# Kernel optimization log

Hardware: AMD Instinct MI355X
Metric: run time of the kernel (lower is better)

Reference implementation:

```python
import jax, jax.numpy as jnp
import numpy as np

N_TIME, N_BATCH, N_STATE, N_FORCE = 64, 8192, 32, 16
DT = 0.05          # implicit (backward-Euler) step size
NEWTON_ITERS = 6   # fixed Newton-Raphson iteration count (converges well below fp32 eps here)


def setup_inputs() -> dict:
    key = jax.random.key(0)
    k = jax.random.split(key, 5)
    return {
        "y0": jax.random.normal(k[0], (N_BATCH, N_STATE), jnp.float32) * 0.1,
        "forces": jax.random.normal(k[1], (N_TIME, N_BATCH, N_FORCE), jnp.float32),
        "W": jax.random.normal(k[2], (N_STATE, N_STATE), jnp.float32) / np.float32(np.sqrt(N_STATE)),
        "U": jax.random.normal(k[3], (N_STATE, N_FORCE), jnp.float32) / np.float32(np.sqrt(N_FORCE)),
        "b": jax.random.normal(k[4], (N_STATE,), jnp.float32) * 0.01,
        "n": N_TIME,
    }


def reference(y0, forces, W, U, b, n):
    """Sequential recursive nonlinear solve, block_size=1, ZeroPredictor guess.

    Each step solves R(y_k) = y_k - y_{k-1} - dt*tanh(W y_k + U u_k + b) = 0
    via Newton-Raphson with a batched dense solve of the diagonal Jacobian
    block J[1] = I - dt*diag(1-t^2) W (the Thomas factorization for a single
    step reduces to this dense solve).
    """
    S = y0.shape[-1]
    I = jnp.eye(S, dtype=y0.dtype)

    def step(y_prev, u):
        fu = u @ U.T + b                      # [B,S] constant per Newton solve
        y = jnp.zeros_like(y_prev)            # ZeroPredictor initial guess
        for _ in range(NEWTON_ITERS):         # plain Newton-Raphson
            t = jnp.tanh(y @ W.T + fu)        # [B,S]
            R = y - y_prev - DT * t           # residual [B,S]
            J = I - DT * ((1.0 - t * t)[..., :, None] * W)  # [B,S,S] dR/dy
            y = y - jnp.linalg.solve(J, R[..., None])[..., 0]
        return y, y

    _, ys = jax.lax.scan(step, y0, forces[1:n])   # sequential recursion over time
    return jnp.concatenate([y0[None], ys], axis=0)  # result[0] = y0
```

## Files before the change

kernel.cpp:

```cpp
#include <hip/hip_runtime.h>

#define NT 64
#define NB 8192
#define NS 32
#define NF 16
#define DT 0.05f

typedef float f32x4 __attribute__((ext_vector_type(4)));
typedef short s16x8 __attribute__((ext_vector_type(8)));

__device__ __forceinline__ void bsplit(float v, unsigned short& hi, unsigned short& lo) {
    unsigned int u = __float_as_uint(v);
    hi = (unsigned short)(u >> 16);
    float rest = v - __uint_as_float(u & 0xFFFF0000u);
    lo = (unsigned short)(__float_as_uint(rest) >> 16);
}

__device__ __forceinline__ void split8(const float* p, s16x8& hi, s16x8& lo) {
#pragma unroll
    for (int e = 0; e < 8; ++e) {
        unsigned short hs, ls;
        bsplit(p[e], hs, ls);
        hi[e] = (short)hs;
        lo[e] = (short)ls;
    }
}

__device__ __forceinline__ float tanh1(float x) {
    const float K = 2.8853900817779268f;
    float e = __builtin_amdgcn_exp2f(K * x);
    float r = __builtin_amdgcn_rcpf(e + 1.0f);
    return fmaf(-2.0f, r, 1.0f);
}

__global__ __launch_bounds__(64) void rnes_kernel(
    const float* __restrict__ y0,
    const float* __restrict__ forces,
    const float* __restrict__ W,
    const float* __restrict__ U,
    const float* __restrict__ bias,
    float* __restrict__ out)
{
    const int lane = threadIdx.x;
    const int m    = lane & 15;
    const int h    = lane >> 4;
    const int gb   = blockIdx.x * 16 + m;

    __shared__ __align__(16) unsigned short Yhi[16 * 40];
    __shared__ __align__(16) unsigned short Ylo[16 * 40];

    s16x8 WA0h, WA0l, WA1h, WA1l;
    split8(W + m * NS + 8 * h,        WA0h, WA0l);
    split8(W + (m + 16) * NS + 8 * h, WA1h, WA1l);

    s16x8 UA0h = {0,0,0,0,0,0,0,0}, UA0l = UA0h, UA1h = UA0h, UA1l = UA0h;
    if (h < 2) {
        split8(U + m * NF + 8 * h,        UA0h, UA0l);
        split8(U + (m + 16) * NF + 8 * h, UA1h, UA1l);
    }

    const f32x4 biasA = *(const f32x4*)(bias + 4 * h);
    const f32x4 biasB = *(const f32x4*)(bias + 16 + 4 * h);

    const float* yb = y0 + (size_t)gb * NS;
    f32x4 ypA = *(const f32x4*)(yb + 4 * h);
    f32x4 ypB = *(const f32x4*)(yb + 16 + 4 * h);
    {
        float* o0 = out + (size_t)gb * NS;
        __builtin_nontemporal_store(ypA, (f32x4*)(o0 + 4 * h));
        __builtin_nontemporal_store(ypB, (f32x4*)(o0 + 16 + 4 * h));
    }
    f32x4 yppA = ypA, yppB = ypB;

    const size_t fstep = (size_t)NB * NF;
    const float* fba = forces + (size_t)gb * NF + 8 * h;
    f32x4 un0 = {0.f,0.f,0.f,0.f}, un1 = un0;
    if (h < 2) {
        un0 = __builtin_nontemporal_load((const f32x4*)(fba + fstep));
        un1 = __builtin_nontemporal_load((const f32x4*)(fba + fstep + 4));
    }

    for (int k = 1; k < NT; ++k) {
        s16x8 Buh = {0,0,0,0,0,0,0,0}, Bul = Buh;
        if (h < 2) {
            float uv[8] = {un0[0],un0[1],un0[2],un0[3],un1[0],un1[1],un1[2],un1[3]};
            split8(uv, Buh, Bul);
        }
        f32x4 fuA = biasA;
        fuA = __builtin_amdgcn_mfma_f32_16x16x32_bf16(UA0l, Buh, fuA, 0, 0, 0);
        fuA = __builtin_amdgcn_mfma_f32_16x16x32_bf16(UA0h, Bul, fuA, 0, 0, 0);
        fuA = __builtin_amdgcn_mfma_f32_16x16x32_bf16(UA0h, Buh, fuA, 0, 0, 0);
        f32x4 fuB = biasB;
        fuB = __builtin_amdgcn_mfma_f32_16x16x32_bf16(UA1l, Buh, fuB, 0, 0, 0);
        fuB = __builtin_amdgcn_mfma_f32_16x16x32_bf16(UA1h, Bul, fuB, 0, 0, 0);
        fuB = __builtin_amdgcn_mfma_f32_16x16x32_bf16(UA1h, Buh, fuB, 0, 0, 0);

        if (h < 2) {
            int kn = (k + 1 < NT) ? (k + 1) : (NT - 1);
            un0 = __builtin_nontemporal_load((const f32x4*)(fba + (size_t)kn * fstep));
            un1 = __builtin_nontemporal_load((const f32x4*)(fba + (size_t)kn * fstep + 4));
        }

        f32x4 yA = ypA + (ypA - yppA);
        f32x4 yB = ypB + (ypB - yppB);

        auto iterate = [&]() {
            unsigned dh0, dh1, dl0, dl1;
            {
                unsigned short h0,h1,h2,h3,l0,l1,l2,l3;
                bsplit(yA[0],h0,l0); bsplit(yA[1],h1,l1);
                bsplit(yA[2],h2,l2); bsplit(yA[3],h3,l3);
                dh0 = (unsigned)h0 | ((unsigned)h1 << 16);
                dh1 = (unsigned)h2 | ((unsigned)h3 << 16);
                dl0 = (unsigned)l0 | ((unsigned)l1 << 16);
                dl1 = (unsigned)l2 | ((unsigned)l3 << 16);
            }
            *reinterpret_cast<unsigned long long*>(&Yhi[m * 40 + 4 * h]) =
                (unsigned long long)dh0 | ((unsigned long long)dh1 << 32);
            *reinterpret_cast<unsigned long long*>(&Ylo[m * 40 + 4 * h]) =
                (unsigned long long)dl0 | ((unsigned long long)dl1 << 32);
            {
                unsigned short h0,h1,h2,h3,l0,l1,l2,l3;
                bsplit(yB[0],h0,l0); bsplit(yB[1],h1,l1);
                bsplit(yB[2],h2,l2); bsplit(yB[3],h3,l3);
                dh0 = (unsigned)h0 | ((unsigned)h1 << 16);
                dh1 = (unsigned)h2 | ((unsigned)h3 << 16);
                dl0 = (unsigned)l0 | ((unsigned)l1 << 16);
                dl1 = (unsigned)l2 | ((unsigned)l3 << 16);
            }
            *reinterpret_cast<unsigned long long*>(&Yhi[m * 40 + 16 + 4 * h]) =
                (unsigned long long)dh0 | ((unsigned long long)dh1 << 32);
            *reinterpret_cast<unsigned long long*>(&Ylo[m * 40 + 16 + 4 * h]) =
                (unsigned long long)dl0 | ((unsigned long long)dl1 << 32);
            asm volatile("" ::: "memory");

            s16x8 Bh = *reinterpret_cast<const s16x8*>(&Yhi[m * 40 + 8 * h]);
            s16x8 Bl = *reinterpret_cast<const s16x8*>(&Ylo[m * 40 + 8 * h]);

            f32x4 zA = fuA;
            zA = __builtin_amdgcn_mfma_f32_16x16x32_bf16(WA0l, Bh, zA, 0, 0, 0);
            zA = __builtin_amdgcn_mfma_f32_16x16x32_bf16(WA0h, Bl, zA, 0, 0, 0);
            zA = __builtin_amdgcn_mfma_f32_16x16x32_bf16(WA0h, Bh, zA, 0, 0, 0);
            f32x4 zB = fuB;
            zB = __builtin_amdgcn_mfma_f32_16x16x32_bf16(WA1l, Bh, zB, 0, 0, 0);
            zB = __builtin_amdgcn_mfma_f32_16x16x32_bf16(WA1h, Bl, zB, 0, 0, 0);
            zB = __builtin_amdgcn_mfma_f32_16x16x32_bf16(WA1h, Bh, zB, 0, 0, 0);

#pragma unroll
            for (int r = 0; r < 4; ++r) {
                yA[r] = fmaf(DT, tanh1(zA[r]), ypA[r]);
                yB[r] = fmaf(DT, tanh1(zB[r]), ypB[r]);
            }
        };
        iterate();
        iterate();
        if (k == 1) iterate();

        yppA = ypA; yppB = ypB;
        ypA = yA;   ypB = yB;

        float* op = out + ((size_t)k * NB + gb) * NS;
        __builtin_nontemporal_store(yA, (f32x4*)(op + 4 * h));
        __builtin_nontemporal_store(yB, (f32x4*)(op + 16 + 4 * h));
    }
}

extern "C" void kernel_launch(void* const* d_in, const int* in_sizes, int n_in,
                              void* d_out, int out_size, void* d_ws, size_t ws_size,
                              hipStream_t stream) {
    const float* y0     = (const float*)d_in[0];
    const float* forces = (const float*)d_in[1];
    const float* W      = (const float*)d_in[2];
    const float* U      = (const float*)d_in[3];
    const float* b      = (const float*)d_in[4];
    float* out = (float*)d_out;

    dim3 grid(NB / 16);
    dim3 block(64);
    rnes_kernel<<<grid, block, 0, stream>>>(y0, forces, W, U, b, out);
}
```

Baseline: 152.1 us.

## Permute W/U rows so MFMA output feeds next B operand in registers

Reorders the rows of W and U assigned to each MFMA output tile so that each lane's accumulator outputs correspond exactly to the 8 contiguous state elements it needs as the B operand of the next Newton iteration. This removes the per-iteration LDS round-trip (stores of hi/lo bf16 splits plus reads) from the serial dependency chain. Output stores and bias loads are remapped to match the new element ownership. It also adds a launch bound of one block per SM hint.

```diff
diff --git a/kernel.cpp b/kernel.cpp
--- a/kernel.cpp
+++ b/kernel.cpp
@@ -33,7 +33,7 @@
     return fmaf(-2.0f, r, 1.0f);
 }
 
-__global__ __launch_bounds__(64) void rnes_kernel(
+__global__ __launch_bounds__(64, 1) void rnes_kernel(
     const float* __restrict__ y0,
     const float* __restrict__ forces,
     const float* __restrict__ W,
@@ -46,29 +46,29 @@
     const int h    = lane >> 4;
     const int gb   = blockIdx.x * 16 + m;
 
-    __shared__ __align__(16) unsigned short Yhi[16 * 40];
-    __shared__ __align__(16) unsigned short Ylo[16 * 40];
+    const int rA = 8 * (m >> 2) + (m & 3);
+    const int rB = rA + 4;
 
-    s16x8 WA0h, WA0l, WA1h, WA1l;
-    split8(W + m * NS + 8 * h,        WA0h, WA0l);
-    split8(W + (m + 16) * NS + 8 * h, WA1h, WA1l);
+    s16x8 WAh, WAl, WBh, WBl;
+    split8(W + rA * NS + 8 * h, WAh, WAl);
+    split8(W + rB * NS + 8 * h, WBh, WBl);
 
-    s16x8 UA0h = {0,0,0,0,0,0,0,0}, UA0l = UA0h, UA1h = UA0h, UA1l = UA0h;
+    s16x8 UAh = {0,0,0,0,0,0,0,0}, UAl = UAh, UBh = UAh, UBl = UAh;
     if (h < 2) {
-        split8(U + m * NF + 8 * h,        UA0h, UA0l);
-        split8(U + (m + 16) * NF + 8 * h, UA1h, UA1l);
+        split8(U + rA * NF + 8 * h, UAh, UAl);
+        split8(U + rB * NF + 8 * h, UBh, UBl);
     }
 
-    const f32x4 biasA = *(const f32x4*)(bias + 4 * h);
-    const f32x4 biasB = *(const f32x4*)(bias + 16 + 4 * h);
+    const f32x4 bvA = *(const f32x4*)(bias + 8 * h);
+    const f32x4 bvB = *(const f32x4*)(bias + 8 * h + 4);
 
-    const float* yb = y0 + (size_t)gb * NS;
-    f32x4 ypA = *(const f32x4*)(yb + 4 * h);
-    f32x4 ypB = *(const f32x4*)(yb + 16 + 4 * h);
+    const float* yb = y0 + (size_t)gb * NS + 8 * h;
+    f32x4 ypA = *(const f32x4*)(yb);
+    f32x4 ypB = *(const f32x4*)(yb + 4);
     {
-        float* o0 = out + (size_t)gb * NS;
-        __builtin_nontemporal_store(ypA, (f32x4*)(o0 + 4 * h));
-        __builtin_nontemporal_store(ypB, (f32x4*)(o0 + 16 + 4 * h));
+        float* o0 = out + (size_t)gb * NS + 8 * h;
+        __builtin_nontemporal_store(ypA, (f32x4*)(o0));
+        __builtin_nontemporal_store(ypB, (f32x4*)(o0 + 4));
     }
     f32x4 yppA = ypA, yppB = ypB;
 
@@ -86,14 +86,14 @@
             float uv[8] = {un0[0],un0[1],un0[2],un0[3],un1[0],un1[1],un1[2],un1[3]};
             split8(uv, Buh, Bul);
         }
-        f32x4 fuA = biasA;
-        fuA = __builtin_amdgcn_mfma_f32_16x16x32_bf16(UA0l, Buh, fuA, 0, 0, 0);
-        fuA = __builtin_amdgcn_mfma_f32_16x16x32_bf16(UA0h, Bul, fuA, 0, 0, 0);
-        fuA = __builtin_amdgcn_mfma_f32_16x16x32_bf16(UA0h, Buh, fuA, 0, 0, 0);
-        f32x4 fuB = biasB;
-        fuB = __builtin_amdgcn_mfma_f32_16x16x32_bf16(UA1l, Buh, fuB, 0, 0, 0);
-        fuB = __builtin_amdgcn_mfma_f32_16x16x32_bf16(UA1h, Bul, fuB, 0, 0, 0);
-        fuB = __builtin_amdgcn_mfma_f32_16x16x32_bf16(UA1h, Buh, fuB, 0, 0, 0);
+        f32x4 fuA = bvA;
+        fuA = __builtin_amdgcn_mfma_f32_16x16x32_bf16(UAl, Buh, fuA, 0, 0, 0);
+        fuA = __builtin_amdgcn_mfma_f32_16x16x32_bf16(UAh, Bul, fuA, 0, 0, 0);
+        fuA = __builtin_amdgcn_mfma_f32_16x16x32_bf16(UAh, Buh, fuA, 0, 0, 0);
+        f32x4 fuB = bvB;
+        fuB = __builtin_amdgcn_mfma_f32_16x16x32_bf16(UBl, Buh, fuB, 0, 0, 0);
+        fuB = __builtin_amdgcn_mfma_f32_16x16x32_bf16(UBh, Bul, fuB, 0, 0, 0);
+        fuB = __builtin_amdgcn_mfma_f32_16x16x32_bf16(UBh, Buh, fuB, 0, 0, 0);
 
         if (h < 2) {
             int kn = (k + 1 < NT) ? (k + 1) : (NT - 1);
@@ -105,46 +105,26 @@
         f32x4 yB = ypB + (ypB - yppB);
 
         auto iterate = [&]() {
-            unsigned dh0, dh1, dl0, dl1;
+            s16x8 Bh, Bl;
             {
-                unsigned short h0,h1,h2,h3,l0,l1,l2,l3;
-                bsplit(yA[0],h0,l0); bsplit(yA[1],h1,l1);
-                bsplit(yA[2],h2,l2); bsplit(yA[3],h3,l3);
-                dh0 = (unsigned)h0 | ((unsigned)h1 << 16);
-                dh1 = (unsigned)h2 | ((unsigned)h3 << 16);
-                dl0 = (unsigned)l0 | ((unsigned)l1 << 16);
-                dl1 = (unsigned)l2 | ((unsigned)l3 << 16);
+                unsigned short hs, ls;
+                bsplit(yA[0], hs, ls); Bh[0] = (short)hs; Bl[0] = (short)ls;
+                bsplit(yA[1], hs, ls); Bh[1] = (short)hs; Bl[1] = (short)ls;
+                bsplit(yA[2], hs, ls); Bh[2] = (short)hs; Bl[2] = (short)ls;
+                bsplit(yA[3], hs, ls); Bh[3] = (short)hs; Bl[3] = (short)ls;
+                bsplit(yB[0], hs, ls); Bh[4] = (short)hs; Bl[4] = (short)ls;
+                bsplit(yB[1], hs, ls); Bh[5] = (short)hs; Bl[5] = (short)ls;
+                bsplit(yB[2], hs, ls); Bh[6] = (short)hs; Bl[6] = (short)ls;
+                bsplit(yB[3], hs, ls); Bh[7] = (short)hs; Bl[7] = (short)ls;
             }
-            *reinterpret_cast<unsigned long long*>(&Yhi[m * 40 + 4 * h]) =
-                (unsigned long long)dh0 | ((unsigned long long)dh1 << 32);
-            *reinterpret_cast<unsigned long long*>(&Ylo[m * 40 + 4 * h]) =
-                (unsigned long long)dl0 | ((unsigned long long)dl1 << 32);
-            {
-                unsigned short h0,h1,h2,h3,l0,l1,l2,l3;
-                bsplit(yB[0],h0,l0); bsplit(yB[1],h1,l1);
-                bsplit(yB[2],h2,l2); bsplit(yB[3],h3,l3);
-                dh0 = (unsigned)h0 | ((unsigned)h1 << 16);
-                dh1 = (unsigned)h2 | ((unsigned)h3 << 16);
-                dl0 = (unsigned)l0 | ((unsigned)l1 << 16);
-                dl1 = (unsigned)l2 | ((unsigned)l3 << 16);
-            }
-            *reinterpret_cast<unsigned long long*>(&Yhi[m * 40 + 16 + 4 * h]) =
-                (unsigned long long)dh0 | ((unsigned long long)dh1 << 32);
-            *reinterpret_cast<unsigned long long*>(&Ylo[m * 40 + 16 + 4 * h]) =
-                (unsigned long long)dl0 | ((unsigned long long)dl1 << 32);
-            asm volatile("" ::: "memory");
-
-            s16x8 Bh = *reinterpret_cast<const s16x8*>(&Yhi[m * 40 + 8 * h]);
-            s16x8 Bl = *reinterpret_cast<const s16x8*>(&Ylo[m * 40 + 8 * h]);
-
             f32x4 zA = fuA;
-            zA = __builtin_amdgcn_mfma_f32_16x16x32_bf16(WA0l, Bh, zA, 0, 0, 0);
-            zA = __builtin_amdgcn_mfma_f32_16x16x32_bf16(WA0h, Bl, zA, 0, 0, 0);
-            zA = __builtin_amdgcn_mfma_f32_16x16x32_bf16(WA0h, Bh, zA, 0, 0, 0);
+            zA = __builtin_amdgcn_mfma_f32_16x16x32_bf16(WAl, Bh, zA, 0, 0, 0);
+            zA = __builtin_amdgcn_mfma_f32_16x16x32_bf16(WAh, Bl, zA, 0, 0, 0);
+            zA = __builtin_amdgcn_mfma_f32_16x16x32_bf16(WAh, Bh, zA, 0, 0, 0);
             f32x4 zB = fuB;
-            zB = __builtin_amdgcn_mfma_f32_16x16x32_bf16(WA1l, Bh, zB, 0, 0, 0);
-            zB = __builtin_amdgcn_mfma_f32_16x16x32_bf16(WA1h, Bl, zB, 0, 0, 0);
-            zB = __builtin_amdgcn_mfma_f32_16x16x32_bf16(WA1h, Bh, zB, 0, 0, 0);
+            zB = __builtin_amdgcn_mfma_f32_16x16x32_bf16(WBl, Bh, zB, 0, 0, 0);
+            zB = __builtin_amdgcn_mfma_f32_16x16x32_bf16(WBh, Bl, zB, 0, 0, 0);
+            zB = __builtin_amdgcn_mfma_f32_16x16x32_bf16(WBh, Bh, zB, 0, 0, 0);
 
 #pragma unroll
             for (int r = 0; r < 4; ++r) {
@@ -159,9 +139,9 @@
         yppA = ypA; yppB = ypB;
         ypA = yA;   ypB = yB;
 
-        float* op = out + ((size_t)k * NB + gb) * NS;
-        __builtin_nontemporal_store(yA, (f32x4*)(op + 4 * h));
-        __builtin_nontemporal_store(yB, (f32x4*)(op + 16 + 4 * h));
+        float* op = out + ((size_t)k * NB + gb) * NS + 8 * h;
+        __builtin_nontemporal_store(yA, (f32x4*)(op));
+        __builtin_nontemporal_store(yB, (f32x4*)(op + 4));
     }
 }
 
```

Result: faster. 144.9 us (-4.7%).
